# Kernel optimization log

Hardware: AMD Instinct MI355X
Metric: run time of the kernel (lower is better)

Reference implementation:

```python
import jax, jax.numpy as jnp
import numpy as np
import math

HIDDEN = 2048
NUM_HEADS = 16
HEAD_DIM = HIDDEN // NUM_HEADS
B, S = 2, 2048


def setup_inputs() -> dict:
    key = jax.random.key(0)
    k1, k2, k3, k4, k5 = jax.random.split(key, 5)
    scale = 1.0 / math.sqrt(HIDDEN)
    return {
        "hidden_states": jax.random.normal(k1, (B, S, HIDDEN), dtype=jnp.float32),
        "attention_mask": jnp.ones((B, S), dtype=jnp.float32),
        "Wq": jax.random.normal(k2, (HIDDEN, HIDDEN), dtype=jnp.float32) * scale,
        "Wk": jax.random.normal(k3, (HEAD_DIM, HIDDEN), dtype=jnp.float32) * scale,
        "Wv": jax.random.normal(k4, (HEAD_DIM, HIDDEN), dtype=jnp.float32) * scale,
        "Wo": jax.random.normal(k5, (HIDDEN, HIDDEN), dtype=jnp.float32) * scale,
    }


def reference(hidden_states, attention_mask, Wq, Wk, Wv, Wo):
    bsz, tgt, _ = hidden_states.shape
    # projections (torch Linear: x @ W.T)
    q = (hidden_states @ Wq.T).reshape(bsz, tgt, NUM_HEADS, HEAD_DIM).transpose(0, 2, 1, 3)  # [B,H,S,D]
    k = (hidden_states @ Wk.T)[:, None, :, :]  # [B,1,S,D] (MQA single KV head)
    v = (hidden_states @ Wv.T)[:, None, :, :]
    # scores with MQA broadcast (no K expand materialization)
    scores = jnp.einsum("bhsd,bokd->bhsk", q, k) / math.sqrt(HEAD_DIM)  # [B,H,S,S]
    neg = jnp.finfo(scores.dtype).min
    scores = scores + (1.0 - attention_mask)[:, None, None, :] * neg
    probs = jax.nn.softmax(scores, axis=-1)
    attn = jnp.einsum("bhsk,bokd->bhsd", probs, v)  # [B,H,S,D]
    out = attn.transpose(0, 2, 1, 3).reshape(bsz, tgt, HIDDEN) @ Wo.T
    # cache returned by the module (expanded to all heads, as in torch code)
    key_states = jnp.broadcast_to(k, (bsz, NUM_HEADS, tgt, HEAD_DIM))
    value_states = jnp.broadcast_to(v, (bsz, NUM_HEADS, tgt, HEAD_DIM))
    return out, key_states, value_states
```

## Files before the change

kernel.cpp:

```cpp
#include <hip/hip_runtime.h>
#include <hip/hip_bf16.h>
#include <math.h>

#define B_   2
#define S_   2048
#define HID  2048
#define NH   16
#define HD   128

typedef __bf16 bf16_t;
typedef __bf16 bf16x4 __attribute__((ext_vector_type(4)));
typedef __bf16 bf16x8 __attribute__((ext_vector_type(8)));
typedef float  f32x4  __attribute__((ext_vector_type(4)));

__device__ __forceinline__ f32x4 mfma16(bf16x8 a, bf16x8 b, f32x4 c) {
    return __builtin_amdgcn_mfma_f32_16x16x32_bf16(a, b, c, 0, 0, 0);
}

__device__ __forceinline__ void gl2lds16(const void* g, void* l) {
    __builtin_amdgcn_global_load_lds((__attribute__((address_space(1))) void*)(g),
                                     (__attribute__((address_space(3))) void*)(l),
                                     16, 0, 0);
}

__global__ void convert_bf16(const float* __restrict__ s0, const float* __restrict__ s1,
                             const float* __restrict__ s2, const float* __restrict__ s3,
                             const float* __restrict__ s4,
                             bf16_t* __restrict__ d0, bf16_t* __restrict__ d1,
                             bf16_t* __restrict__ d2, bf16_t* __restrict__ d3,
                             bf16_t* __restrict__ d4)
{
    const size_t stride = (size_t)gridDim.x * blockDim.x;
    for (size_t i = (size_t)blockIdx.x * blockDim.x + threadIdx.x; i < 4325376; i += stride) {
        const float* s; bf16_t* d; size_t off;
        if (i < 2097152)      { s = s0; d = d0; off = i; }
        else if (i < 3145728) { s = s1; d = d1; off = i - 2097152; }
        else if (i < 3211264) { s = s2; d = d2; off = i - 3145728; }
        else if (i < 3276800) { s = s3; d = d3; off = i - 3211264; }
        else                  { s = s4; d = d4; off = i - 3276800; }
        float4 v = ((const float4*)s)[off];
        bf16x4 o;
        o[0] = (bf16_t)v.x; o[1] = (bf16_t)v.y; o[2] = (bf16_t)v.z; o[3] = (bf16_t)v.w;
        ((bf16x4*)d)[off] = o;
    }
}

__global__ void broadcast_kv(const bf16_t* __restrict__ k_ws, const bf16_t* __restrict__ v_ws,
                             float* __restrict__ keyo, float* __restrict__ valo)
{
    const size_t stride = (size_t)gridDim.x * blockDim.x;
    for (size_t i = (size_t)blockIdx.x * blockDim.x + threadIdx.x; i < 4194304; i += stride) {
        int which = i >= 2097152;
        size_t f = which ? i - 2097152 : i;
        size_t e = f * 4;
        int d = (int)(e & 127);
        size_t s = (e >> 7) & 2047;
        size_t b = e >> 22;
        const bf16_t* src = (which ? v_ws : k_ws) + (b * S_ + s) * HD + d;
        bf16x4 kv = *(const bf16x4*)src;
        float4 o;
        o.x = (float)kv[0]; o.y = (float)kv[1]; o.z = (float)kv[2]; o.w = (float)kv[3];
        *(float4*)((which ? valo : keyo) + e) = o;
    }
}

template <int MODE>
__global__ __launch_bounds__(256, 2)
void gemm_nt(const bf16_t* __restrict__ A,  const bf16_t* __restrict__ B0,
             const bf16_t* __restrict__ B1, const bf16_t* __restrict__ B2,
             bf16_t* __restrict__ q_ws, bf16_t* __restrict__ k_ws,
             bf16_t* __restrict__ v_ws, bf16_t* __restrict__ vt_ws,
             float* __restrict__ outf)
{
    __shared__ __align__(16) ushort sA[128 * 32];
    __shared__ __align__(16) ushort sB[128 * 32];

    const int tid  = threadIdx.x;
    const int lane = tid & 63;
    const int wave = tid >> 6;
    const int quad = lane >> 4;
    const int l16  = lane & 15;
    const int bn = blockIdx.x, bm = blockIdx.y;
    const int wm = (wave & 1) * 64;
    const int wn = (wave >> 1) * 64;

    const bf16_t* Bbase;
    if (MODE == 0) Bbase = (bn < 16) ? (B0 + (size_t)bn * 128 * HID) : (bn == 16 ? B1 : B2);
    else           Bbase = B0 + (size_t)bn * 128 * HID;
    const bf16_t* Abase = A + (size_t)bm * 128 * HID;

    const int c0 = tid, c1 = tid + 256;
    const int r0 = c0 >> 2, o0 = (c0 & 3) * 8;
    const int r1 = c1 >> 2, o1 = (c1 & 3) * 8;

    f32x4 acc[4][4] = {};

    for (int kt = 0; kt < HID / 32; ++kt) {
        const int ko = kt * 32;
        gl2lds16(Abase + (size_t)r0 * HID + ko + o0, sA + c0 * 8);
        gl2lds16(Abase + (size_t)r1 * HID + ko + o1, sA + c1 * 8);
        gl2lds16(Bbase + (size_t)r0 * HID + ko + o0, sB + c0 * 8);
        gl2lds16(Bbase + (size_t)r1 * HID + ko + o1, sB + c1 * 8);
        __syncthreads();

        bf16x8 af[4], bfr[4];
        for (int mt = 0; mt < 4; ++mt)
            af[mt] = *(const bf16x8*)(sA + (wm + mt * 16 + l16) * 32 + quad * 8);
        for (int nt = 0; nt < 4; ++nt)
            bfr[nt] = *(const bf16x8*)(sB + (wn + nt * 16 + l16) * 32 + quad * 8);
        for (int mt = 0; mt < 4; ++mt)
            for (int nt = 0; nt < 4; ++nt)
                acc[mt][nt] = mfma16(af[mt], bfr[nt], acc[mt][nt]);
        __syncthreads();
    }

    for (int mt = 0; mt < 4; ++mt) {
        for (int nt = 0; nt < 4; ++nt) {
            for (int j = 0; j < 4; ++j) {
                float v = acc[mt][nt][j];
                int row = bm * 128 + wm + mt * 16 + quad * 4 + j;
                int col = wn + nt * 16 + l16;
                if (MODE == 1) {
                    outf[(size_t)row * HID + bn * 128 + col] = v;
                } else {
                    bf16_t bv = (bf16_t)v;
                    if (bn < 16) {
                        q_ws[(size_t)row * HID + bn * 128 + col] = bv;
                    } else {
                        int b = row >> 11, s = row & 2047, d = col;
                        if (bn == 16) {
                            k_ws[((size_t)b * S_ + s) * HD + d] = bv;
                        } else {
                            v_ws[((size_t)b * S_ + s) * HD + d] = bv;
                            vt_ws[((size_t)b * HD + d) * S_ + s] = bv;
                        }
                    }
                }
            }
        }
    }
}

#define SV_U 9216
#define SM_U 18432

__global__ __launch_bounds__(256, 2)
void attn_kernel(const bf16_t* __restrict__ Qw, const bf16_t* __restrict__ Kc,
                 const bf16_t* __restrict__ Vt, const float* __restrict__ mask,
                 bf16_t* __restrict__ Ow)
{
    __shared__ __align__(16) ushort smem[18560];
    float* sMask = (float*)&smem[SM_U];

    const int tid  = threadIdx.x;
    const int lane = tid & 63;
    const int wave = tid >> 6;
    const int quad = lane >> 4;
    const int l16  = lane & 15;
    const int qt = blockIdx.x;
    const int bh = blockIdx.y;
    const int b = bh >> 4, h = bh & 15;

    const bf16_t* kg = Kc + (size_t)b * S_ * HD;
    const bf16_t* vg = Vt + (size_t)b * HD * S_;

    bf16x8 qf[2][4];
    {
        const bf16_t* qg = Qw + ((size_t)(b * S_ + qt * 128 + wave * 32)) * HID + h * HD;
#pragma unroll
        for (int mt = 0; mt < 2; ++mt)
#pragma unroll
            for (int kk = 0; kk < 4; ++kk)
                qf[mt][kk] = *(const bf16x8*)(qg + (size_t)(mt * 16 + l16) * HID + kk * 32 + quad * 8);
    }

    f32x4 oa[2][8] = {};
    float mrow[2][4], lrow[2][4];
#pragma unroll
    for (int mt = 0; mt < 2; ++mt)
#pragma unroll
        for (int j = 0; j < 4; ++j) { mrow[mt][j] = -INFINITY; lrow[mt][j] = 0.f; }

    const float scale2 = 0.08838834764831845f * 1.4426950408889634f;
    const float NEGF   = -3.4028234663852886e38f;
    const float LOG2E  = 1.4426950408889634f;

    for (int kt = 0; kt < S_ / 64; ++kt) {
        __syncthreads();
        {
            uint4 kr[4], vr[4];
#pragma unroll
            for (int i = 0; i < 4; ++i) {
                int c = tid + i * 256;
                kr[i] = *(const uint4*)(kg + (size_t)(kt * 64 + (c >> 4)) * HD + (c & 15) * 8);
                vr[i] = *(const uint4*)(vg + (size_t)(c >> 3) * S_ + kt * 64 + (c & 7) * 8);
            }
#pragma unroll
            for (int i = 0; i < 4; ++i) {
                int c = tid + i * 256;
                *(uint4*)(&smem[(c >> 4) * 136 + (c & 15) * 8]) = kr[i];
                *(uint4*)(&smem[SV_U + (c >> 3) * 72 + (c & 7) * 8]) = vr[i];
            }
        }
        if (tid < 64) {
            float mv = mask[b * S_ + kt * 64 + tid];
            sMask[tid] = (1.0f - mv) * NEGF * LOG2E;
        }
        __syncthreads();

        f32x4 sa[2][4] = {};
#pragma unroll
        for (int kk = 0; kk < 4; ++kk)
#pragma unroll
            for (int nt = 0; nt < 4; ++nt) {
                bf16x8 kf = *(const bf16x8*)(&smem[(nt * 16 + l16) * 136 + kk * 32 + quad * 8]);
#pragma unroll
                for (int mt = 0; mt < 2; ++mt)
                    sa[mt][nt] = mfma16(qf[mt][kk], kf, sa[mt][nt]);
            }
#pragma unroll
        for (int nt = 0; nt < 4; ++nt) {
            float madd = sMask[nt * 16 + l16];
#pragma unroll
            for (int mt = 0; mt < 2; ++mt)
#pragma unroll
                for (int j = 0; j < 4; ++j)
                    sa[mt][nt][j] = sa[mt][nt][j] * scale2 + madd;
        }
        __syncthreads();

        float rm[2][4];
#pragma unroll
        for (int mt = 0; mt < 2; ++mt)
#pragma unroll
            for (int j = 0; j < 4; ++j) {
                float m = sa[mt][0][j];
#pragma unroll
                for (int nt = 1; nt < 4; ++nt) m = fmaxf(m, sa[mt][nt][j]);
                rm[mt][j] = m;
            }
#pragma unroll
        for (int off = 1; off < 16; off <<= 1)
#pragma unroll
            for (int mt = 0; mt < 2; ++mt)
#pragma unroll
                for (int j = 0; j < 4; ++j)
                    rm[mt][j] = fmaxf(rm[mt][j], __shfl_xor(rm[mt][j], off));
        bool need = false;
#pragma unroll
        for (int mt = 0; mt < 2; ++mt)
#pragma unroll
            for (int j = 0; j < 4; ++j)
                need = need || (rm[mt][j] > mrow[mt][j] + 8.0f);
        if (__any((int)need)) {
#pragma unroll
            for (int mt = 0; mt < 2; ++mt)
#pragma unroll
                for (int j = 0; j < 4; ++j) {
                    float mnew  = fmaxf(mrow[mt][j], rm[mt][j]);
                    float alpha = exp2f(mrow[mt][j] - mnew);
                    mrow[mt][j] = mnew;
                    lrow[mt][j] *= alpha;
#pragma unroll
                    for (int nt = 0; nt < 8; ++nt) oa[mt][nt][j] *= alpha;
                }
        }
        bf16_t* sPp = (bf16_t*)&smem[wave * 2304];
#pragma unroll
        for (int mt = 0; mt < 2; ++mt) {
            float rs[4] = {0.f, 0.f, 0.f, 0.f};
#pragma unroll
            for (int nt = 0; nt < 4; ++nt)
#pragma unroll
                for (int j = 0; j < 4; ++j) {
                    float p = exp2f(sa[mt][nt][j] - mrow[mt][j]);
                    rs[j] += p;
                    sPp[(mt * 16 + quad * 4 + j) * 72 + nt * 16 + l16] = (bf16_t)p;
                }
#pragma unroll
            for (int off = 1; off < 16; off <<= 1)
#pragma unroll
                for (int j = 0; j < 4; ++j) rs[j] += __shfl_xor(rs[j], off);
#pragma unroll
            for (int j = 0; j < 4; ++j) lrow[mt][j] += rs[j];
        }

        bf16x8 pf[2][2];
#pragma unroll
        for (int mt = 0; mt < 2; ++mt)
#pragma unroll
            for (int kk = 0; kk < 2; ++kk)
                pf[mt][kk] = *(const bf16x8*)(&smem[wave * 2304 + (mt * 16 + l16) * 72 + kk * 32 + quad * 8]);
#pragma unroll
        for (int kk = 0; kk < 2; ++kk)
#pragma unroll
            for (int nt = 0; nt < 8; ++nt) {
                bf16x8 vf = *(const bf16x8*)(&smem[SV_U + (nt * 16 + l16) * 72 + kk * 32 + quad * 8]);
#pragma unroll
                for (int mt = 0; mt < 2; ++mt)
                    oa[mt][nt] = mfma16(pf[mt][kk], vf, oa[mt][nt]);
            }
    }

#pragma unroll
    for (int mt = 0; mt < 2; ++mt)
#pragma unroll
        for (int j = 0; j < 4; ++j) {
            float inv = 1.0f / lrow[mt][j];
            int s = qt * 128 + wave * 32 + mt * 16 + quad * 4 + j;
#pragma unroll
            for (int nt = 0; nt < 8; ++nt) {
                int d = nt * 16 + l16;
                Ow[((size_t)(b * S_ + s)) * HID + h * HD + d] = (bf16_t)(oa[mt][nt][j] * inv);
            }
        }
}

extern "C" void kernel_launch(void* const* d_in, const int* in_sizes, int n_in,
                              void* d_out, int out_size, void* d_ws, size_t ws_size,
                              hipStream_t stream) {
    const float* hs   = (const float*)d_in[0];
    const float* mask = (const float*)d_in[1];
    const float* Wq   = (const float*)d_in[2];
    const float* Wk   = (const float*)d_in[3];
    const float* Wv   = (const float*)d_in[4];
    const float* Wo   = (const float*)d_in[5];
    float* out = (float*)d_out;

    bf16_t* wqb = (bf16_t*)out;
    bf16_t* wkb = wqb + 4194304;
    bf16_t* wvb = wkb + 262144;
    bf16_t* qb  = (bf16_t*)(out + 8388608);
    bf16_t* wob = (bf16_t*)(out + 12582912);
    bf16_t* hsb = (bf16_t*)(out + 16777216);
    bf16_t* o_ws = hsb;

    bf16_t* k_ws  = (bf16_t*)d_ws;
    bf16_t* v_ws  = k_ws + 524288;
    bf16_t* vt_ws = v_ws + 524288;

    convert_bf16<<<2048, 256, 0, stream>>>(hs, Wq, Wk, Wv, Wo, hsb, wqb, wkb, wvb, wob);
    gemm_nt<0><<<dim3(18, 32), 256, 0, stream>>>(hsb, wqb, wkb, wvb, qb, k_ws, v_ws, vt_ws, nullptr);
    attn_kernel<<<dim3(16, 32), 256, 0, stream>>>(qb, k_ws, vt_ws, mask, o_ws);
    gemm_nt<1><<<dim3(16, 32), 256, 0, stream>>>(o_ws, wob, nullptr, nullptr, nullptr, nullptr, nullptr, nullptr, out);
    broadcast_kv<<<4096, 256, 0, stream>>>(k_ws, v_ws, out + 8388608, out + 16777216);
}
```

Measured before the change: 415.2 us.

## Compute transposed QK^T scores, keep P in registers, swizzle LDS tiles

The QK^T MFMA operands are swapped so each lane holds scores for a single query row. Row max and row sum then need two cross-quad shuffles instead of a 16-lane butterfly. The P tile is no longer written to and read back from LDS; it is rearranged into the PV MFMA operand layout with lane shuffles, which also removes one __syncthreads per iteration. K and V tiles use XOR-swizzled unpadded LDS rows in place of padding, which shrinks shared memory but adds shuffle work and more complex indexing.

```diff
diff --git a/kernel.cpp b/kernel.cpp
--- a/kernel.cpp
+++ b/kernel.cpp
@@ -12,6 +12,7 @@
 typedef __bf16 bf16x4 __attribute__((ext_vector_type(4)));
 typedef __bf16 bf16x8 __attribute__((ext_vector_type(8)));
 typedef float  f32x4  __attribute__((ext_vector_type(4)));
+typedef unsigned int u32x4 __attribute__((ext_vector_type(4)));
 
 __device__ __forceinline__ f32x4 mfma16(bf16x8 a, bf16x8 b, f32x4 c) {
     return __builtin_amdgcn_mfma_f32_16x16x32_bf16(a, b, c, 0, 0, 0);
@@ -21,6 +22,12 @@
     __builtin_amdgcn_global_load_lds((__attribute__((address_space(1))) void*)(g),
                                      (__attribute__((address_space(3))) void*)(l),
                                      16, 0, 0);
+}
+
+__device__ __forceinline__ unsigned int pkbf(float a, float b) {
+    unsigned short ua = __builtin_bit_cast(unsigned short, (bf16_t)a);
+    unsigned short ub = __builtin_bit_cast(unsigned short, (bf16_t)b);
+    return (unsigned int)ua | ((unsigned int)ub << 16);
 }
 
 __global__ void convert_bf16(const float* __restrict__ s0, const float* __restrict__ s1,
@@ -141,15 +148,15 @@
     }
 }
 
-#define SV_U 9216
-#define SM_U 18432
+#define SV_U 8192
+#define SM_U 16384
 
 __global__ __launch_bounds__(256, 2)
 void attn_kernel(const bf16_t* __restrict__ Qw, const bf16_t* __restrict__ Kc,
                  const bf16_t* __restrict__ Vt, const float* __restrict__ mask,
                  bf16_t* __restrict__ Ow)
 {
-    __shared__ __align__(16) ushort smem[18560];
+    __shared__ __align__(16) ushort smem[16512];
     float* sMask = (float*)&smem[SM_U];
 
     const int tid  = threadIdx.x;
@@ -175,11 +182,8 @@
     }
 
     f32x4 oa[2][8] = {};
-    float mrow[2][4], lrow[2][4];
-#pragma unroll
-    for (int mt = 0; mt < 2; ++mt)
-#pragma unroll
-        for (int j = 0; j < 4; ++j) { mrow[mt][j] = -INFINITY; lrow[mt][j] = 0.f; }
+    float mrow[2] = { -INFINITY, -INFINITY };
+    float lrow[2] = { 0.f, 0.f };
 
     const float scale2 = 0.08838834764831845f * 1.4426950408889634f;
     const float NEGF   = -3.4028234663852886e38f;
@@ -198,8 +202,10 @@
 #pragma unroll
             for (int i = 0; i < 4; ++i) {
                 int c = tid + i * 256;
-                *(uint4*)(&smem[(c >> 4) * 136 + (c & 15) * 8]) = kr[i];
-                *(uint4*)(&smem[SV_U + (c >> 3) * 72 + (c & 7) * 8]) = vr[i];
+                int krow = c >> 4, kchk = c & 15;
+                *(uint4*)(&smem[krow * 128 + ((kchk ^ (krow & 7)) << 3)]) = kr[i];
+                int vrow = c >> 3, vchk = c & 7;
+                *(uint4*)(&smem[SV_U + vrow * 64 + ((vchk ^ (vrow & 7)) << 3)]) = vr[i];
             }
         }
         if (tid < 64) {
@@ -213,89 +219,100 @@
         for (int kk = 0; kk < 4; ++kk)
 #pragma unroll
             for (int nt = 0; nt < 4; ++nt) {
-                bf16x8 kf = *(const bf16x8*)(&smem[(nt * 16 + l16) * 136 + kk * 32 + quad * 8]);
+                bf16x8 kf = *(const bf16x8*)(&smem[(nt * 16 + l16) * 128 + (((4 * kk + quad) ^ (l16 & 7)) << 3)]);
 #pragma unroll
                 for (int mt = 0; mt < 2; ++mt)
-                    sa[mt][nt] = mfma16(qf[mt][kk], kf, sa[mt][nt]);
+                    sa[mt][nt] = mfma16(kf, qf[mt][kk], sa[mt][nt]);
             }
 #pragma unroll
         for (int nt = 0; nt < 4; ++nt) {
-            float madd = sMask[nt * 16 + l16];
+            f32x4 m4 = *(const f32x4*)&sMask[nt * 16 + quad * 4];
 #pragma unroll
             for (int mt = 0; mt < 2; ++mt)
 #pragma unroll
                 for (int j = 0; j < 4; ++j)
-                    sa[mt][nt][j] = sa[mt][nt][j] * scale2 + madd;
-        }
-        __syncthreads();
-
-        float rm[2][4];
-#pragma unroll
-        for (int mt = 0; mt < 2; ++mt)
-#pragma unroll
-            for (int j = 0; j < 4; ++j) {
-                float m = sa[mt][0][j];
-#pragma unroll
-                for (int nt = 1; nt < 4; ++nt) m = fmaxf(m, sa[mt][nt][j]);
-                rm[mt][j] = m;
-            }
-#pragma unroll
-        for (int off = 1; off < 16; off <<= 1)
-#pragma unroll
-            for (int mt = 0; mt < 2; ++mt)
+                    sa[mt][nt][j] = sa[mt][nt][j] * scale2 + m4[j];
+        }
+
+        float rm[2];
+#pragma unroll
+        for (int mt = 0; mt < 2; ++mt) {
+            float m = sa[mt][0][0];
+#pragma unroll
+            for (int nt = 0; nt < 4; ++nt)
 #pragma unroll
                 for (int j = 0; j < 4; ++j)
-                    rm[mt][j] = fmaxf(rm[mt][j], __shfl_xor(rm[mt][j], off));
-        bool need = false;
-#pragma unroll
-        for (int mt = 0; mt < 2; ++mt)
-#pragma unroll
-            for (int j = 0; j < 4; ++j)
-                need = need || (rm[mt][j] > mrow[mt][j] + 8.0f);
+                    m = fmaxf(m, sa[mt][nt][j]);
+            m = fmaxf(m, __shfl_xor(m, 16));
+            m = fmaxf(m, __shfl_xor(m, 32));
+            rm[mt] = m;
+        }
+        bool need = (rm[0] > mrow[0] + 8.0f) || (rm[1] > mrow[1] + 8.0f);
         if (__any((int)need)) {
 #pragma unroll
-            for (int mt = 0; mt < 2; ++mt)
+            for (int mt = 0; mt < 2; ++mt) {
+                float mnew  = fmaxf(mrow[mt], rm[mt]);
+                float alpha = exp2f(mrow[mt] - mnew);
+                mrow[mt] = mnew;
+                lrow[mt] *= alpha;
 #pragma unroll
                 for (int j = 0; j < 4; ++j) {
-                    float mnew  = fmaxf(mrow[mt][j], rm[mt][j]);
-                    float alpha = exp2f(mrow[mt][j] - mnew);
-                    mrow[mt][j] = mnew;
-                    lrow[mt][j] *= alpha;
-#pragma unroll
-                    for (int nt = 0; nt < 8; ++nt) oa[mt][nt][j] *= alpha;
+                    float aj = __shfl(alpha, (lane & 48) | (quad * 4 + j));
+#pragma unroll
+                    for (int nt = 0; nt < 8; ++nt) oa[mt][nt][j] *= aj;
                 }
-        }
-        bf16_t* sPp = (bf16_t*)&smem[wave * 2304];
+            }
+        }
+        unsigned int g[2][4][2];
 #pragma unroll
         for (int mt = 0; mt < 2; ++mt) {
-            float rs[4] = {0.f, 0.f, 0.f, 0.f};
-#pragma unroll
-            for (int nt = 0; nt < 4; ++nt)
-#pragma unroll
-                for (int j = 0; j < 4; ++j) {
-                    float p = exp2f(sa[mt][nt][j] - mrow[mt][j]);
-                    rs[j] += p;
-                    sPp[(mt * 16 + quad * 4 + j) * 72 + nt * 16 + l16] = (bf16_t)p;
+            float rs = 0.f;
+#pragma unroll
+            for (int nt = 0; nt < 4; ++nt) {
+                float p0 = exp2f(sa[mt][nt][0] - mrow[mt]);
+                float p1 = exp2f(sa[mt][nt][1] - mrow[mt]);
+                float p2 = exp2f(sa[mt][nt][2] - mrow[mt]);
+                float p3 = exp2f(sa[mt][nt][3] - mrow[mt]);
+                rs += (p0 + p1) + (p2 + p3);
+                g[mt][nt][0] = pkbf(p0, p1);
+                g[mt][nt][1] = pkbf(p2, p3);
+            }
+            rs += __shfl_xor(rs, 16);
+            rs += __shfl_xor(rs, 32);
+            lrow[mt] += rs;
+        }
+
+        bf16x8 pf[2][2];
+        {
+            const int sl = ((quad & 1) << 5) + l16;
+            const int sh = sl + 16;
+            const bool hi = (quad & 2) != 0;
+#pragma unroll
+            for (int kk = 0; kk < 2; ++kk)
+#pragma unroll
+                for (int mt = 0; mt < 2; ++mt) {
+                    unsigned int a0 = __shfl(g[mt][2 * kk][0], sl);
+                    unsigned int a1 = __shfl(g[mt][2 * kk][1], sl);
+                    unsigned int b0 = __shfl(g[mt][2 * kk + 1][0], sl);
+                    unsigned int b1 = __shfl(g[mt][2 * kk + 1][1], sl);
+                    unsigned int c0 = __shfl(g[mt][2 * kk][0], sh);
+                    unsigned int c1 = __shfl(g[mt][2 * kk][1], sh);
+                    unsigned int d0 = __shfl(g[mt][2 * kk + 1][0], sh);
+                    unsigned int d1 = __shfl(g[mt][2 * kk + 1][1], sh);
+                    u32x4 w;
+                    w[0] = hi ? b0 : a0;
+                    w[1] = hi ? b1 : a1;
+                    w[2] = hi ? d0 : c0;
+                    w[3] = hi ? d1 : c1;
+                    pf[mt][kk] = __builtin_bit_cast(bf16x8, w);
                 }
-#pragma unroll
-            for (int off = 1; off < 16; off <<= 1)
-#pragma unroll
-                for (int j = 0; j < 4; ++j) rs[j] += __shfl_xor(rs[j], off);
-#pragma unroll
-            for (int j = 0; j < 4; ++j) lrow[mt][j] += rs[j];
-        }
-
-        bf16x8 pf[2][2];
-#pragma unroll
-        for (int mt = 0; mt < 2; ++mt)
-#pragma unroll
-            for (int kk = 0; kk < 2; ++kk)
-                pf[mt][kk] = *(const bf16x8*)(&smem[wave * 2304 + (mt * 16 + l16) * 72 + kk * 32 + quad * 8]);
+        }
+
 #pragma unroll
         for (int kk = 0; kk < 2; ++kk)
 #pragma unroll
             for (int nt = 0; nt < 8; ++nt) {
-                bf16x8 vf = *(const bf16x8*)(&smem[SV_U + (nt * 16 + l16) * 72 + kk * 32 + quad * 8]);
+                bf16x8 vf = *(const bf16x8*)(&smem[SV_U + (nt * 16 + l16) * 64 + (((4 * kk + quad) ^ (l16 & 7)) << 3)]);
 #pragma unroll
                 for (int mt = 0; mt < 2; ++mt)
                     oa[mt][nt] = mfma16(pf[mt][kk], vf, oa[mt][nt]);
@@ -306,7 +323,8 @@
     for (int mt = 0; mt < 2; ++mt)
 #pragma unroll
         for (int j = 0; j < 4; ++j) {
-            float inv = 1.0f / lrow[mt][j];
+            float lv = __shfl(lrow[mt], (lane & 48) | (quad * 4 + j));
+            float inv = 1.0f / lv;
             int s = qt * 128 + wave * 32 + mt * 16 + quad * 4 + j;
 #pragma unroll
             for (int nt = 0; nt < 8; ++nt) {
```

New measurement: 422.1 us. Within noise of the previous version (+1.7%).
